# Performance work log

Measured on AMD Instinct MI355X. Metric: run time of the kernel, lower is better.

## Reference

```python
import jax, jax.numpy as jnp
import numpy as np

K = 7          # neighborhood kernel size (7x7)
NH = 8         # num heads


def _nbr_idx(n):
    # NATTEN-style clamped windows: window start = clip(i - K//2, 0, n-K)
    pos = jnp.arange(n)
    start = jnp.clip(pos - K // 2, 0, n - K)          # (n,)
    idx = start[:, None] + jnp.arange(K)[None, :]     # (n, K) absolute key positions
    rel = idx - pos[:, None] + (K - 1)                # (n, K) in [0, 2K-2] for rpb lookup
    return idx, rel


def _forward(x, w_qkv, b_qkv, rpb, w_proj, b_proj, w_fc1, b_fc1, w_fc2, b_fc2):
    B, C, H, W = x.shape
    hd = C // NH
    scale = hd ** -0.5

    # ---- neighborhood attention (norm0 = Identity) ----
    xp = jnp.transpose(x, (0, 2, 3, 1))                           # (B,H,W,C)
    qkv = xp @ w_qkv + b_qkv                                      # (B,H,W,3C)
    qkv = qkv.reshape(B, H, W, 3, NH, hd)
    q = qkv[:, :, :, 0] * scale                                   # (B,H,W,nh,hd)
    k = qkv[:, :, :, 1]
    v = qkv[:, :, :, 2]

    idx_h, rel_h = _nbr_idx(H)                                    # (H,K)
    idx_w, rel_w = _nbr_idx(W)                                    # (W,K)

    # gather 7x7 neighborhoods: (B,H,K,W,K,nh,hd)
    k_nbr = k[:, idx_h][:, :, :, idx_w]
    v_nbr = v[:, idx_h][:, :, :, idx_w]

    # attention logits: (B,H,W,nh,K,K)
    attn = jnp.einsum('bxynd,bxiyjnd->bxynij', q, k_nbr)
    # relative positional bias: rpb (nh, 2K-1, 2K-1) -> (nh,H,K,W,K)
    bias = rpb[:, rel_h][:, :, :, rel_w]                          # (nh,H,K,W,K)
    attn = attn + jnp.transpose(bias, (1, 3, 0, 2, 4))[None]      # (B,H,W,nh,K,K)

    attn = jax.nn.softmax(attn.reshape(B, H, W, NH, K * K), axis=-1)
    attn = attn.reshape(B, H, W, NH, K, K)

    out = jnp.einsum('bxynij,bxiyjnd->bxynd', attn, v_nbr)        # (B,H,W,nh,hd)
    out = out.reshape(B, H, W, C) @ w_proj + b_proj               # (B,H,W,C)
    x1 = jnp.transpose(out, (0, 3, 1, 2)) + x                     # residual skip0

    # ---- MLP (1x1-conv style, channels-first; norm1 = Identity) ----
    h = jnp.einsum('bchw,cf->bfhw', x1, w_fc1) + b_fc1[None, :, None, None]
    h = jax.nn.gelu(h, approximate=False)                         # torch nn.GELU (erf)
    y = jnp.einsum('bfhw,fc->bchw', h, w_fc2) + b_fc2[None, :, None, None]
    return y + x1                                                 # residual skip1


def setup_inputs() -> dict:
    key = jax.random.key(0)
    B, C, H, W = 1, 256, 64, 128
    hid = int(C * 2.0)
    ks = jax.random.split(key, 8)
    s = 0.02
    return {
        'x': jax.random.normal(ks[0], (B, C, H, W), jnp.float32),
        'w_qkv': jax.random.normal(ks[1], (C, 3 * C), jnp.float32) * s,
        'b_qkv': jnp.zeros((3 * C,), jnp.float32),
        'rpb': jax.random.normal(ks[2], (NH, 2 * K - 1, 2 * K - 1), jnp.float32) * s,
        'w_proj': jax.random.normal(ks[3], (C, C), jnp.float32) * s,
        'b_proj': jnp.zeros((C,), jnp.float32),
        'w_fc1': jax.random.normal(ks[4], (C, hid), jnp.float32) * s,
        'b_fc1': jnp.zeros((hid,), jnp.float32),
        'w_fc2': jax.random.normal(ks[5], (hid, C), jnp.float32) * s,
        'b_fc2': jnp.zeros((C,), jnp.float32),
    }


def reference(x, w_qkv, b_qkv, rpb, w_proj, b_proj, w_fc1, b_fc1, w_fc2, b_fc2):
    return _forward(x, w_qkv, b_qkv, rpb, w_proj, b_proj, w_fc1, b_fc1, w_fc2, b_fc2)
```

## Files before the change

kernel.cpp:

```cpp
#include <hip/hip_runtime.h>

typedef unsigned short ushort;
typedef short bf16x8 __attribute__((ext_vector_type(8)));
typedef float f32x4 __attribute__((ext_vector_type(4)));

static __device__ __forceinline__ ushort f2b(float f) {
  unsigned u = __builtin_bit_cast(unsigned, f);
  u = (u + 0x7fffu + ((u >> 16) & 1u)) >> 16;
  return (ushort)u;
}
static __device__ __forceinline__ float b2f(ushort b) {
  return __builtin_bit_cast(float, (unsigned)b << 16);
}

__global__ __launch_bounds__(256) void prep_kernel(
    const float* __restrict__ x,
    const float* __restrict__ w_qkv, const float* __restrict__ w_proj,
    const float* __restrict__ w_fc1, const float* __restrict__ w_fc2,
    ushort* __restrict__ xb, ushort* __restrict__ wqkvT,
    ushort* __restrict__ wprojT, ushort* __restrict__ wfc1T,
    ushort* __restrict__ wfc2T)
{
  __shared__ float tile[32][33];
  int t = blockIdx.x;
  const float* src; ushort* dst; int R, Nc, r0, c0;
  if (t < 2048)              { src = x;      dst = xb;     R = 256; Nc = 8192; r0 = (t >> 8) * 32; c0 = (t & 255) * 32; }
  else if ((t -= 2048) < 192){ src = w_qkv;  dst = wqkvT;  R = 256; Nc = 768;  r0 = (t / 24) * 32; c0 = (t % 24) * 32; }
  else if ((t -= 192) < 64)  { src = w_proj; dst = wprojT; R = 256; Nc = 256;  r0 = (t / 8) * 32;  c0 = (t % 8) * 32; }
  else if ((t -= 64) < 128)  { src = w_fc1;  dst = wfc1T;  R = 256; Nc = 512;  r0 = (t / 16) * 32; c0 = (t % 16) * 32; }
  else           { t -= 128;   src = w_fc2;  dst = wfc2T;  R = 512; Nc = 256;  r0 = (t / 8) * 32;  c0 = (t % 8) * 32; }

  const int tx = threadIdx.x & 31, ty = threadIdx.x >> 5;
  #pragma unroll
  for (int i = 0; i < 4; i++)
    tile[ty + i * 8][tx] = src[(size_t)(r0 + ty + i * 8) * Nc + c0 + tx];
  __syncthreads();
  #pragma unroll
  for (int i = 0; i < 4; i++)
    dst[(size_t)(c0 + ty + i * 8) * R + r0 + tx] = f2b(tile[tx][ty + i * 8]);
}

template<int EPI>
__global__ __launch_bounds__(256) void gemm_mfma(
    const ushort* __restrict__ A, const ushort* __restrict__ Bt,
    const float* __restrict__ bias, const float* __restrict__ R,
    const ushort* __restrict__ RS,
    void* __restrict__ C0, void* __restrict__ C1,
    int M, int N, int K)
{
  __shared__ __attribute__((aligned(16))) ushort As[64 * 40];
  __shared__ __attribute__((aligned(16))) ushort Bs[64 * 40];

  const int bm = blockIdx.y * 64;
  const int bn = blockIdx.x * 64;
  const int t  = threadIdx.x;
  const int w    = t >> 6;
  const int lane = t & 63;
  const int wm = (w & 1) * 32;
  const int wn = (w >> 1) * 32;
  const int lm = lane & 15;
  const int kq = lane >> 4;

  const int sm = t >> 2;
  const int sk = (t & 3) * 8;

  f32x4 acc[2][2] = {};

  for (int k0 = 0; k0 < K; k0 += 32) {
    *(uint4*)(&As[sm * 40 + sk]) = *(const uint4*)(A  + (size_t)(bm + sm) * K + k0 + sk);
    *(uint4*)(&Bs[sm * 40 + sk]) = *(const uint4*)(Bt + (size_t)(bn + sm) * K + k0 + sk);
    __syncthreads();

    bf16x8 a0 = *(const bf16x8*)(&As[(wm + lm)      * 40 + kq * 8]);
    bf16x8 a1 = *(const bf16x8*)(&As[(wm + 16 + lm) * 40 + kq * 8]);
    bf16x8 b0 = *(const bf16x8*)(&Bs[(wn + lm)      * 40 + kq * 8]);
    bf16x8 b1 = *(const bf16x8*)(&Bs[(wn + 16 + lm) * 40 + kq * 8]);
    acc[0][0] = __builtin_amdgcn_mfma_f32_16x16x32_bf16(a0, b0, acc[0][0], 0, 0, 0);
    acc[0][1] = __builtin_amdgcn_mfma_f32_16x16x32_bf16(a0, b1, acc[0][1], 0, 0, 0);
    acc[1][0] = __builtin_amdgcn_mfma_f32_16x16x32_bf16(a1, b0, acc[1][0], 0, 0, 0);
    acc[1][1] = __builtin_amdgcn_mfma_f32_16x16x32_bf16(a1, b1, acc[1][1], 0, 0, 0);
    __syncthreads();
  }

  #pragma unroll
  for (int ti = 0; ti < 2; ti++) {
    #pragma unroll
    for (int tj = 0; tj < 2; tj++) {
      const int n  = bn + wn + tj * 16 + lm;
      const int m0 = bm + wm + ti * 16 + kq * 4;
      if (EPI == 3) {
        float4 v;
        float* vp = &v.x;
        #pragma unroll
        for (int r = 0; r < 4; r++)
          vp[r] = acc[ti][tj][r] + bias[n] + b2f(RS[(size_t)(m0 + r) * 256 + n]);
        *(float4*)((float*)C0 + (size_t)n * M + m0) = v;
      } else if (EPI == 0) {
        if (n < 512) {
          #pragma unroll
          for (int r = 0; r < 4; r++)
            ((ushort*)C0)[(size_t)(m0 + r) * N + n] = f2b(acc[ti][tj][r] + bias[n]);
        } else {
          ushort4 st;
          st.x = f2b(acc[ti][tj][0] + bias[n]);
          st.y = f2b(acc[ti][tj][1] + bias[n]);
          st.z = f2b(acc[ti][tj][2] + bias[n]);
          st.w = f2b(acc[ti][tj][3] + bias[n]);
          *(ushort4*)((ushort*)C1 + (size_t)(n - 512) * 8192 + m0) = st;
        }
      } else {
        #pragma unroll
        for (int r = 0; r < 4; r++) {
          const int m = m0 + r;
          float v = acc[ti][tj][r] + bias[n];
          if (EPI == 1) {
            v += R[(size_t)n * M + m];
            ((ushort*)C0)[(size_t)m * 256 + n] = f2b(v);
          } else {
            v = 0.5f * v * (1.0f + erff(v * 0.70710678118f));
            ((ushort*)C0)[(size_t)m * N + n] = f2b(v);
          }
        }
      }
    }
  }
}

__global__ __launch_bounds__(256) void natt_mfma(
    const ushort* __restrict__ qkv, const ushort* __restrict__ vT,
    const float* __restrict__ rpb, ushort* __restrict__ att)
{
  __shared__ __attribute__((aligned(16))) ushort Plds[4][7][16][40];
  __shared__ float Rlds[4][176];

  const int w    = threadIdx.x >> 6;
  const int lane = threadIdx.x & 63;
  const int l  = lane & 15;
  const int q  = lane >> 4;
  const int tile = blockIdx.x;
  const int n    = blockIdx.y * 4 + w;
  const int ph  = tile >> 3;
  const int pw0 = (tile & 7) << 4;
  const int p0  = ph * 128 + pw0;

  int sh = ph - 3;  sh = sh < 0 ? 0 : (sh > 57 ? 57 : sh);
  int sb = pw0 - 3; sb = sb < 0 ? 0 : sb;
  const int sba = sb & ~7;

  const float L2E = 1.44269504f;
  for (int idx = lane; idx < 169; idx += 64)
    Rlds[w][idx] = rpb[n * 169 + idx] * L2E;

  bf16x8 qf = *(const bf16x8*)(qkv + (size_t)(p0 + l) * 768 + n * 32 + q * 8);

  f32x4 s[7][2] = {};
  #pragma unroll
  for (int i = 0; i < 7; i++) {
    const int rowp = (sh + i) * 128;
    #pragma unroll
    for (int h = 0; h < 2; h++) {
      int jc = sba + h * 16 + l;
      jc = jc > 127 ? 127 : jc;
      bf16x8 kf = *(const bf16x8*)(qkv + (size_t)(rowp + jc) * 768 + 256 + n * 32 + q * 8);
      s[i][h] = __builtin_amdgcn_mfma_f32_16x16x32_bf16(qf, kf, s[i][h], 0, 0, 0);
    }
  }
  __syncthreads();

  const float KSC = 0.17677669529663689f * 1.44269504f;
  const int relh0 = sh - ph + 6;
  float rsum[4] = {0.f, 0.f, 0.f, 0.f};
  #pragma unroll
  for (int r = 0; r < 4; r++) {
    const int pw = pw0 + q * 4 + r;
    int sw = pw - 3; sw = sw < 0 ? 0 : (sw > 121 ? 121 : sw);
    #pragma unroll
    for (int h = 0; h < 2; h++) {
      const int jc = sba + h * 16 + l;
      const bool valid = (unsigned)(jc - sw) <= 6u;
      int relw = jc - pw + 6;
      relw = relw < 0 ? 0 : (relw > 12 ? 12 : relw);
      #pragma unroll
      for (int i = 0; i < 7; i++) {
        float b = Rlds[w][(relh0 + i) * 13 + relw];
        float v = s[i][h][r] * KSC + b;
        v = valid ? v : -1e30f;
        float e = exp2f(v);
        s[i][h][r] = e;
        rsum[r] += e;
      }
    }
  }
  #pragma unroll
  for (int r = 0; r < 4; r++) {
    rsum[r] += __shfl_xor(rsum[r], 1);
    rsum[r] += __shfl_xor(rsum[r], 2);
    rsum[r] += __shfl_xor(rsum[r], 4);
    rsum[r] += __shfl_xor(rsum[r], 8);
  }

  #pragma unroll
  for (int i = 0; i < 7; i++)
    #pragma unroll
    for (int h = 0; h < 2; h++)
      #pragma unroll
      for (int r = 0; r < 4; r++)
        Plds[w][i][q * 4 + r][h * 16 + l] = f2b(s[i][h][r]);
  __syncthreads();

  f32x4 o[2] = {};
  #pragma unroll
  for (int i = 0; i < 7; i++) {
    bf16x8 pf = *(const bf16x8*)(&Plds[w][i][l][q * 8]);
    const int rowp = (sh + i) * 128;
    #pragma unroll
    for (int dh = 0; dh < 2; dh++) {
      bf16x8 vf = *(const bf16x8*)(vT + (size_t)(n * 32 + dh * 16 + l) * 8192
                                      + rowp + sba + q * 8);
      o[dh] = __builtin_amdgcn_mfma_f32_16x16x32_bf16(pf, vf, o[dh], 0, 0, 0);
    }
  }

  #pragma unroll
  for (int r = 0; r < 4; r++) {
    const float inv = 1.0f / rsum[r];
    #pragma unroll
    for (int dh = 0; dh < 2; dh++)
      att[(size_t)(p0 + q * 4 + r) * 256 + n * 32 + dh * 16 + l] = f2b(o[dh][r] * inv);
  }
}

extern "C" void kernel_launch(void* const* d_in, const int* in_sizes, int n_in,
                              void* d_out, int out_size, void* d_ws, size_t ws_size,
                              hipStream_t stream)
{
  const float* x      = (const float*)d_in[0];
  const float* w_qkv  = (const float*)d_in[1];
  const float* b_qkv  = (const float*)d_in[2];
  const float* rpb    = (const float*)d_in[3];
  const float* w_proj = (const float*)d_in[4];
  const float* b_proj = (const float*)d_in[5];
  const float* w_fc1  = (const float*)d_in[6];
  const float* b_fc1  = (const float*)d_in[7];
  const float* w_fc2  = (const float*)d_in[8];
  const float* b_fc2  = (const float*)d_in[9];
  float* out = (float*)d_out;

  const int M = 8192;
  char* ws = (char*)d_ws;
  ushort* xb     = (ushort*)(ws);
  ushort* qkv    = (ushort*)(ws + 4194304);
  ushort* x1b    = (ushort*)(ws + 16777216);
  ushort* wqkvT  = (ushort*)(ws + 20971520);
  ushort* wprojT = (ushort*)(ws + 21364736);
  ushort* wfc1T  = (ushort*)(ws + 21495808);
  ushort* wfc2T  = (ushort*)(ws + 21757952);
  ushort* vT     = (ushort*)(ws + 22020096);
  ushort* att = xb;
  ushort* h   = qkv;

  dim3 blk(256);

  prep_kernel<<<dim3(2560), blk, 0, stream>>>(
      x, w_qkv, w_proj, w_fc1, w_fc2, xb, wqkvT, wprojT, wfc1T, wfc2T);

  gemm_mfma<0><<<dim3(768 / 64, M / 64), blk, 0, stream>>>(
      xb, wqkvT, b_qkv, nullptr, nullptr, qkv, vT, M, 768, 256);

  natt_mfma<<<dim3(512, 2), blk, 0, stream>>>(qkv, vT, rpb, att);

  gemm_mfma<1><<<dim3(256 / 64, M / 64), blk, 0, stream>>>(
      att, wprojT, b_proj, x, nullptr, x1b, nullptr, M, 256, 256);

  gemm_mfma<2><<<dim3(512 / 64, M / 64), blk, 0, stream>>>(
      x1b, wfc1T, b_fc1, nullptr, nullptr, h, nullptr, M, 512, 256);

  gemm_mfma<3><<<dim3(256 / 64, M / 64), blk, 0, stream>>>(
      h, wfc2T, b_fc2, nullptr, x1b, out, nullptr, M, 256, 512);
}
```

Baseline: 142.5 us.

## Replace LDS-tiled GEMM with per-wave direct-load MFMA GEMM and larger wave tiles

The shared-memory tiled GEMM, with its two barriers per 32-wide K step, is replaced by a kernel where each wave independently loads its A and B fragments straight from global memory into registers and runs MFMA. Each wave now owns a FI×16 by 64 output tile, and K is a compile-time constant so the loop can be unrolled. Launch grids are recomputed so the four waves of a block cover independent tiles. This removes LDS staging and barrier stalls, but gives up data sharing between waves of a block, relying on L1/L2 to absorb the repeated global reads, and increases register pressure.

```diff
diff --git a/kernel.cpp b/kernel.cpp
--- a/kernel.cpp
+++ b/kernel.cpp
@@ -40,79 +40,78 @@
     dst[(size_t)(c0 + ty + i * 8) * R + r0 + tx] = f2b(tile[tx][ty + i * 8]);
 }
 
-template<int EPI>
-__global__ __launch_bounds__(256) void gemm_mfma(
+template<int EPI, int FI, int KD>
+__global__ __launch_bounds__(256) void gemm_direct(
     const ushort* __restrict__ A, const ushort* __restrict__ Bt,
     const float* __restrict__ bias, const float* __restrict__ R,
     const ushort* __restrict__ RS,
     void* __restrict__ C0, void* __restrict__ C1,
-    int M, int N, int K)
-{
-  __shared__ __attribute__((aligned(16))) ushort As[64 * 40];
-  __shared__ __attribute__((aligned(16))) ushort Bs[64 * 40];
-
-  const int bm = blockIdx.y * 64;
-  const int bn = blockIdx.x * 64;
-  const int t  = threadIdx.x;
-  const int w    = t >> 6;
-  const int lane = t & 63;
-  const int wm = (w & 1) * 32;
-  const int wn = (w >> 1) * 32;
+    int M, int N)
+{
+  const int w    = threadIdx.x >> 6;
+  const int lane = threadIdx.x & 63;
   const int lm = lane & 15;
   const int kq = lane >> 4;
-
-  const int sm = t >> 2;
-  const int sk = (t & 3) * 8;
-
-  f32x4 acc[2][2] = {};
-
-  for (int k0 = 0; k0 < K; k0 += 32) {
-    *(uint4*)(&As[sm * 40 + sk]) = *(const uint4*)(A  + (size_t)(bm + sm) * K + k0 + sk);
-    *(uint4*)(&Bs[sm * 40 + sk]) = *(const uint4*)(Bt + (size_t)(bn + sm) * K + k0 + sk);
-    __syncthreads();
-
-    bf16x8 a0 = *(const bf16x8*)(&As[(wm + lm)      * 40 + kq * 8]);
-    bf16x8 a1 = *(const bf16x8*)(&As[(wm + 16 + lm) * 40 + kq * 8]);
-    bf16x8 b0 = *(const bf16x8*)(&Bs[(wn + lm)      * 40 + kq * 8]);
-    bf16x8 b1 = *(const bf16x8*)(&Bs[(wn + 16 + lm) * 40 + kq * 8]);
-    acc[0][0] = __builtin_amdgcn_mfma_f32_16x16x32_bf16(a0, b0, acc[0][0], 0, 0, 0);
-    acc[0][1] = __builtin_amdgcn_mfma_f32_16x16x32_bf16(a0, b1, acc[0][1], 0, 0, 0);
-    acc[1][0] = __builtin_amdgcn_mfma_f32_16x16x32_bf16(a1, b0, acc[1][0], 0, 0, 0);
-    acc[1][1] = __builtin_amdgcn_mfma_f32_16x16x32_bf16(a1, b1, acc[1][1], 0, 0, 0);
-    __syncthreads();
-  }
-
-  #pragma unroll
-  for (int ti = 0; ti < 2; ti++) {
-    #pragma unroll
-    for (int tj = 0; tj < 2; tj++) {
-      const int n  = bn + wn + tj * 16 + lm;
-      const int m0 = bm + wm + ti * 16 + kq * 4;
+  const int Mtn = M / (FI * 16);
+  const int gw  = blockIdx.x * 4 + w;
+  const int nt  = gw / Mtn;
+  const int mt  = gw % Mtn;
+  const int m0  = mt * FI * 16;
+  const int n0  = nt * 64;
+
+  const ushort* aBase = A  + (size_t)(m0 + lm) * KD + kq * 8;
+  const ushort* bBase = Bt + (size_t)(n0 + lm) * KD + kq * 8;
+
+  f32x4 acc[FI][4] = {};
+
+  #pragma unroll 2
+  for (int k0 = 0; k0 < KD; k0 += 32) {
+    bf16x8 af[FI], bfr[4];
+    #pragma unroll
+    for (int fi = 0; fi < FI; fi++)
+      af[fi] = *(const bf16x8*)(aBase + (size_t)fi * 16 * KD + k0);
+    #pragma unroll
+    for (int fj = 0; fj < 4; fj++)
+      bfr[fj] = *(const bf16x8*)(bBase + (size_t)fj * 16 * KD + k0);
+    #pragma unroll
+    for (int fi = 0; fi < FI; fi++)
+      #pragma unroll
+      for (int fj = 0; fj < 4; fj++)
+        acc[fi][fj] = __builtin_amdgcn_mfma_f32_16x16x32_bf16(
+            af[fi], bfr[fj], acc[fi][fj], 0, 0, 0);
+  }
+
+  #pragma unroll
+  for (int fi = 0; fi < FI; fi++) {
+    #pragma unroll
+    for (int fj = 0; fj < 4; fj++) {
+      const int n  = n0 + fj * 16 + lm;
+      const int mr = m0 + fi * 16 + kq * 4;
       if (EPI == 3) {
         float4 v;
         float* vp = &v.x;
         #pragma unroll
         for (int r = 0; r < 4; r++)
-          vp[r] = acc[ti][tj][r] + bias[n] + b2f(RS[(size_t)(m0 + r) * 256 + n]);
-        *(float4*)((float*)C0 + (size_t)n * M + m0) = v;
+          vp[r] = acc[fi][fj][r] + bias[n] + b2f(RS[(size_t)(mr + r) * 256 + n]);
+        *(float4*)((float*)C0 + (size_t)n * M + mr) = v;
       } else if (EPI == 0) {
         if (n < 512) {
           #pragma unroll
           for (int r = 0; r < 4; r++)
-            ((ushort*)C0)[(size_t)(m0 + r) * N + n] = f2b(acc[ti][tj][r] + bias[n]);
+            ((ushort*)C0)[(size_t)(mr + r) * N + n] = f2b(acc[fi][fj][r] + bias[n]);
         } else {
           ushort4 st;
-          st.x = f2b(acc[ti][tj][0] + bias[n]);
-          st.y = f2b(acc[ti][tj][1] + bias[n]);
-          st.z = f2b(acc[ti][tj][2] + bias[n]);
-          st.w = f2b(acc[ti][tj][3] + bias[n]);
-          *(ushort4*)((ushort*)C1 + (size_t)(n - 512) * 8192 + m0) = st;
+          st.x = f2b(acc[fi][fj][0] + bias[n]);
+          st.y = f2b(acc[fi][fj][1] + bias[n]);
+          st.z = f2b(acc[fi][fj][2] + bias[n]);
+          st.w = f2b(acc[fi][fj][3] + bias[n]);
+          *(ushort4*)((ushort*)C1 + (size_t)(n - 512) * 8192 + mr) = st;
         }
       } else {
         #pragma unroll
         for (int r = 0; r < 4; r++) {
-          const int m = m0 + r;
-          float v = acc[ti][tj][r] + bias[n];
+          const int m = mr + r;
+          float v = acc[fi][fj][r] + bias[n];
           if (EPI == 1) {
             v += R[(size_t)n * M + m];
             ((ushort*)C0)[(size_t)m * 256 + n] = f2b(v);
@@ -264,17 +263,17 @@
   prep_kernel<<<dim3(2560), blk, 0, stream>>>(
       x, w_qkv, w_proj, w_fc1, w_fc2, xb, wqkvT, wprojT, wfc1T, wfc2T);
 
-  gemm_mfma<0><<<dim3(768 / 64, M / 64), blk, 0, stream>>>(
-      xb, wqkvT, b_qkv, nullptr, nullptr, qkv, vT, M, 768, 256);
+  gemm_direct<0, 4, 256><<<dim3(384), blk, 0, stream>>>(
+      xb, wqkvT, b_qkv, nullptr, nullptr, qkv, vT, M, 768);
 
   natt_mfma<<<dim3(512, 2), blk, 0, stream>>>(qkv, vT, rpb, att);
 
-  gemm_mfma<1><<<dim3(256 / 64, M / 64), blk, 0, stream>>>(
-      att, wprojT, b_proj, x, nullptr, x1b, nullptr, M, 256, 256);
-
-  gemm_mfma<2><<<dim3(512 / 64, M / 64), blk, 0, stream>>>(
-      x1b, wfc1T, b_fc1, nullptr, nullptr, h, nullptr, M, 512, 256);
-
-  gemm_mfma<3><<<dim3(256 / 64, M / 64), blk, 0, stream>>>(
-      h, wfc2T, b_fc2, nullptr, x1b, out, nullptr, M, 256, 512);
-}
+  gemm_direct<1, 2, 256><<<dim3(256), blk, 0, stream>>>(
+      att, wprojT, b_proj, x, nullptr, x1b, nullptr, M, 256);
+
+  gemm_direct<2, 4, 256><<<dim3(256), blk, 0, stream>>>(
+      x1b, wfc1T, b_fc1, nullptr, nullptr, h, nullptr, M, 512);
+
+  gemm_direct<3, 2, 512><<<dim3(256), blk, 0, stream>>>(
+      h, wfc2T, b_fc2, nullptr, x1b, out, nullptr, M, 256);
+}
```

Result: slower. 161.2 us (+13.2%).
